# Kernel tuning notes

Measured on AMD Instinct MI355X. Metric: run time of the kernel, lower is better.

Reference implementation:

```python
import jax, jax.numpy as jnp
import numpy as np

D_MODEL = 1024
N_HEADS = 16
HEAD_DIM = D_MODEL // N_HEADS


def setup_inputs() -> dict:
    key = jax.random.key(0)
    ks = jax.random.split(key, 9)
    B, S = 2, 2048
    s = 1.0 / np.sqrt(D_MODEL)
    x = jax.random.normal(ks[0], (B, S, D_MODEL), dtype=jnp.float32)
    Wq = jax.random.normal(ks[1], (N_HEADS, D_MODEL, HEAD_DIM), dtype=jnp.float32) * s
    Wk = jax.random.normal(ks[2], (N_HEADS, D_MODEL, HEAD_DIM), dtype=jnp.float32) * s
    Wv = jax.random.normal(ks[3], (N_HEADS, D_MODEL, HEAD_DIM), dtype=jnp.float32) * s
    bq = jax.random.normal(ks[4], (N_HEADS, HEAD_DIM), dtype=jnp.float32) * s
    bk = jax.random.normal(ks[5], (N_HEADS, HEAD_DIM), dtype=jnp.float32) * s
    bv = jax.random.normal(ks[6], (N_HEADS, HEAD_DIM), dtype=jnp.float32) * s
    Wp = jax.random.normal(ks[7], (D_MODEL, D_MODEL), dtype=jnp.float32) * s
    bp = jax.random.normal(ks[8], (D_MODEL,), dtype=jnp.float32) * s
    return {"x": x, "Wq": Wq, "Wk": Wk, "Wv": Wv, "bq": bq, "bk": bk, "bv": bv, "Wp": Wp, "bp": bp}


def reference(x, Wq, Wk, Wv, bq, bk, bv, Wp, bp):
    # Per-head projections batched over heads: [B,S,D] x [H,D,E] -> [B,H,S,E]
    Q = jnp.einsum('bsd,hde->bhse', x, Wq) + bq[None, :, None, :]
    K = jnp.einsum('bsd,hde->bhse', x, Wk) + bk[None, :, None, :]
    V = jnp.einsum('bsd,hde->bhse', x, Wv) + bv[None, :, None, :]
    scores = jnp.einsum('bhse,bhte->bhst', Q, K) / jnp.sqrt(jnp.asarray(HEAD_DIM, x.dtype))
    attn = jax.nn.softmax(scores, axis=-1)          # [B,H,S,S]
    out = jnp.einsum('bhst,bhte->bhse', attn, V)    # [B,H,S,E]
    B, H, S, E = out.shape
    concat = out.transpose(0, 2, 1, 3).reshape(B, S, H * E)  # concat heads along feature
    return concat @ Wp.T + bp
```

## Files before the change

### kernel.cpp

```cpp
#include <hip/hip_runtime.h>
#include <hip/hip_bf16.h>

typedef __attribute__((ext_vector_type(8))) short short8;
typedef __attribute__((ext_vector_type(4))) short svec4;
typedef __attribute__((ext_vector_type(4))) float float4_t;
typedef __attribute__((ext_vector_type(8))) _Float16 half8;

#define D_MODEL 1024
#define N_HEADS 16
#define HEAD_DIM 64
#define B_SZ 2
#define SEQ 2048
#define M_ROWS (B_SZ*SEQ)
#define NQKV 3072
#define SC_LOG2E 0.18033688011112042f

__device__ __forceinline__ unsigned short f2bf(float f) {
  unsigned u = __float_as_uint(f);
  u += 0x7FFFu + ((u >> 16) & 1u);
  return (unsigned short)(u >> 16);
}

__device__ __forceinline__ unsigned short f2h(float f) {
  _Float16 h = (_Float16)f;
  return *(unsigned short*)&h;
}

__device__ __forceinline__ void gl_lds16(const unsigned short* g, unsigned short* l) {
  __builtin_amdgcn_global_load_lds(
      (const __attribute__((address_space(1))) unsigned int*)(size_t)g,
      (__attribute__((address_space(3))) unsigned int*)(unsigned int)(size_t)l,
      16, 0, 0);
}

__global__ void prep(const float* __restrict__ x, const float* __restrict__ Wp,
                     const float* __restrict__ Wq, const float* __restrict__ Wk,
                     const float* __restrict__ Wv,
                     unsigned short* __restrict__ xb, unsigned short* __restrict__ Wpb,
                     unsigned short* __restrict__ Wall) {
  __shared__ float t[16][17];
  int bid = blockIdx.x;
  if (bid < 5120) {
    const float* src; unsigned short* dst; int base;
    if (bid < 4096) { src = x;  dst = xb;  base = bid * 1024 + threadIdx.x * 4; }
    else            { src = Wp; dst = Wpb; base = (bid - 4096) * 1024 + threadIdx.x * 4; }
    float4 v = *(const float4*)(src + base);
    dst[base + 0] = f2bf(v.x);
    dst[base + 1] = f2bf(v.y);
    dst[base + 2] = f2bf(v.z);
    dst[base + 3] = f2bf(v.w);
  } else {
    int u = bid - 5120;
    int sel = u >> 12;
    u &= 4095;
    const float* W = sel == 0 ? Wq : (sel == 1 ? Wk : Wv);
    int d0 = (u & 63) * 16, e0 = ((u >> 6) & 3) * 16, hh = u >> 8;
    int tx = threadIdx.x & 15, ty = threadIdx.x >> 4;
    t[ty][tx] = W[hh * (D_MODEL * HEAD_DIM) + (d0 + ty) * HEAD_DIM + e0 + tx];
    __syncthreads();
    Wall[(size_t)(sel * 1024 + hh * 64 + e0 + ty) * D_MODEL + d0 + tx] = f2bf(t[tx][ty]);
  }
}

__global__ __launch_bounds__(256) void qkv_gemm(const unsigned short* __restrict__ xb,
                                                const unsigned short* __restrict__ Wall,
                                                const float* __restrict__ bq,
                                                const float* __restrict__ bk,
                                                const float* __restrict__ bv,
                                                unsigned short* __restrict__ Qb,
                                                unsigned short* __restrict__ Kb,
                                                unsigned short* __restrict__ Vtb) {
  __shared__ unsigned short As[128 * 32], Bs[128 * 32];
  __shared__ __align__(16) unsigned short Stage[4][16 * 72];
  const int m0 = blockIdx.x * 128, n0 = blockIdx.y * 128;
  const int lane = threadIdx.x & 63, w = threadIdx.x >> 6;
  const int l16 = lane & 15, quad = lane >> 4;
  const int wm = w & 1, wn = w >> 1;
  const int ldrow = lane >> 2, ldcol = (lane & 3) * 8;
  const unsigned short* ga0 = xb + (size_t)(m0 + w * 32 + ldrow) * D_MODEL + ldcol;
  const unsigned short* ga1 = ga0 + 16 * D_MODEL;
  const unsigned short* gb0 = Wall + (size_t)(n0 + w * 32 + ldrow) * D_MODEL + ldcol;
  const unsigned short* gb1 = gb0 + 16 * D_MODEL;
  unsigned short* lA0 = As + (w * 2 + 0) * 512;
  unsigned short* lA1 = As + (w * 2 + 1) * 512;
  unsigned short* lB0 = Bs + (w * 2 + 0) * 512;
  unsigned short* lB1 = Bs + (w * 2 + 1) * 512;
  float4_t acc[4][4];
  float4_t z = {0.f, 0.f, 0.f, 0.f};
#pragma unroll
  for (int i = 0; i < 4; i++)
#pragma unroll
    for (int j = 0; j < 4; j++) acc[i][j] = z;
  for (int k0 = 0; k0 < D_MODEL; k0 += 32) {
    __syncthreads();
    gl_lds16(ga0 + k0, lA0);
    gl_lds16(ga1 + k0, lA1);
    gl_lds16(gb0 + k0, lB0);
    gl_lds16(gb1 + k0, lB1);
    __syncthreads();
    short8 af[4], bf[4];
#pragma unroll
    for (int i = 0; i < 4; i++) af[i] = *(const short8*)&As[(wm * 64 + i * 16 + l16) * 32 + quad * 8];
#pragma unroll
    for (int j = 0; j < 4; j++) bf[j] = *(const short8*)&Bs[(wn * 64 + j * 16 + l16) * 32 + quad * 8];
#pragma unroll
    for (int i = 0; i < 4; i++)
#pragma unroll
      for (int j = 0; j < 4; j++)
        acc[i][j] = __builtin_amdgcn_mfma_f32_16x16x32_bf16(af[i], bf[j], acc[i][j], 0, 0, 0);
  }
  const int nb = n0 + wn * 64;
  const int sel = nb >> 10;
  const int h = (nb >> 6) & 15;
  const float* bias = sel == 0 ? bq : (sel == 1 ? bk : bv);
  const int mbase = m0 + wm * 64;
  const int bb = mbase >> 11;
  const size_t bh = (size_t)(bb * N_HEADS + h);
  if (sel == 2) {
    unsigned short* vs = &Stage[w][0];
    const size_t vbase = bh * (32 * 4096) + (size_t)((mbase >> 6) & 31) * 4096;
    const int e8 = lane >> 3, ch = lane & 7;
#pragma unroll
    for (int j = 0; j < 4; j++) {
      float be = bias[h * 64 + j * 16 + l16];
#pragma unroll
      for (int i = 0; i < 4; i++)
#pragma unroll
        for (int r = 0; r < 4; r++)
          vs[l16 * 72 + i * 16 + quad * 4 + r] = f2h(acc[i][j][r] + be);
#pragma unroll
      for (int rd = 0; rd < 2; rd++) {
        int er = rd * 8 + e8;
        short8 val = *(const short8*)(vs + er * 72 + ch * 8);
        *(short8*)(Vtb + vbase + (size_t)(j * 16 + er) * 64 + ch * 8) = val;
      }
    }
  } else {
    unsigned short* st = &Stage[w][0];
    unsigned short* dst = (sel == 0) ? Qb : Kb;
    const float qsc = (sel == 0) ? SC_LOG2E : 1.0f;
    const size_t rowbase = bh * SEQ + (mbase & (SEQ - 1));
    const int r2 = lane >> 1, c2 = lane & 1;
#pragma unroll
    for (int j = 0; j < 4; j++) {
      float be = bias[h * 64 + j * 16 + l16];
#pragma unroll
      for (int i = 0; i < 4; i++)
#pragma unroll
        for (int r = 0; r < 4; r++)
          st[(i * 16 + quad * 4 + r) * 18 + l16] = f2bf((acc[i][j][r] + be) * qsc);
#pragma unroll
      for (int p = 0; p < 2; p++) {
        int row = p * 32 + r2;
        short8 val = *(const short8*)(st + row * 18 + c2 * 8);
        *(short8*)(dst + (rowbase + row) * HEAD_DIM + j * 16 + c2 * 8) = val;
      }
    }
  }
}

__global__ __launch_bounds__(512) void attn_kernel(const unsigned short* __restrict__ Q,
                                                   const unsigned short* __restrict__ K,
                                                   const unsigned short* __restrict__ Vt,
                                                   unsigned short* __restrict__ concat) {
  __shared__ __align__(16) union ShU {
    unsigned short kv[2][4][64 * 64];
    struct { float4_t ot[4][4][4][16][4]; float ls[4][4][16]; } c;
  } sh;
  const int b = blockIdx.z, h = blockIdx.y;
  const int tid = threadIdx.x;
  const int lane = tid & 63, w = tid >> 6;
  const int g = w >> 2, wq = w & 3;
  const int l16 = lane & 15, quad = lane >> 4;
  const size_t bh = (size_t)(b * N_HEADS + h);
  const int q0 = blockIdx.x * 256 + wq * 64;
  const int tb = g * 1024;
  float4_t z = {0.f, 0.f, 0.f, 0.f};

  short8 aq[4][2];
#pragma unroll
  for (int rg = 0; rg < 4; rg++)
#pragma unroll
    for (int hf = 0; hf < 2; hf++)
      aq[rg][hf] = *(const short8*)(Q + (bh * SEQ + q0 + rg * 16 + l16) * HEAD_DIM + hf * 32 + quad * 8);

  const int tl = tid & 255;
  const int krow = tl >> 2, kch = (tl & 3) * 8;
  const unsigned short* kg = K + (bh * SEQ + tb + krow) * HEAD_DIM + kch;
  const int swz = (krow & 7) << 3;
  const int ktw0 = (krow * 64 + kch) ^ swz;
  const int ktw1 = (krow * 64 + kch + 32) ^ swz;
  const int vt0 = (tl & 3) * 16, vt1 = vt0 + 8;
  const unsigned short* vg = Vt + bh * (32 * 4096) + (size_t)(tb >> 6) * 4096 + krow * 64 + vt0;
  const int tp0 = ((vt0 >> 5) << 5) + (((vt0 >> 2) & 3) << 3) + (((vt0 >> 4) & 1) << 2);
  const int tp1 = ((vt1 >> 5) << 5) + (((vt1 >> 2) & 3) << 3) + (((vt1 >> 4) & 1) << 2);
  const int vtwA = (krow * 64 + tp0) ^ swz;
  const int vtwB = (krow * 64 + tp0 + 8) ^ swz;
  const int vtwC = (krow * 64 + tp1) ^ swz;
  const int vtwD = (krow * 64 + tp1 + 8) ^ swz;
  const int rsw = (l16 & 7) << 3;

  float4_t o[4][4];
#pragma unroll
  for (int rg = 0; rg < 4; rg++)
#pragma unroll
    for (int ne = 0; ne < 4; ne++) o[rg][ne] = z;
  float lsp[4] = {0.f, 0.f, 0.f, 0.f};

  short8 kreg0 = *(const short8*)kg;
  short8 kreg1 = *(const short8*)(kg + 32);
  short8 vreg0 = *(const short8*)vg;
  short8 vreg1 = *(const short8*)(vg + 8);
  kg += 4096; vg += 4096;

  auto step = [&](unsigned short* kb, unsigned short* vb, int itv) {
    *(short8*)(kb + ktw0) = kreg0;
    *(short8*)(kb + ktw1) = kreg1;
    svec4 a0 = {vreg0[0], vreg0[1], vreg0[2], vreg0[3]};
    svec4 a1 = {vreg0[4], vreg0[5], vreg0[6], vreg0[7]};
    svec4 b0 = {vreg1[0], vreg1[1], vreg1[2], vreg1[3]};
    svec4 b1 = {vreg1[4], vreg1[5], vreg1[6], vreg1[7]};
    *(svec4*)(vb + vtwA) = a0;
    *(svec4*)(vb + vtwB) = a1;
    *(svec4*)(vb + vtwC) = b0;
    *(svec4*)(vb + vtwD) = b1;
    __syncthreads();
    if (itv < 15) {
      kreg0 = *(const short8*)kg;
      kreg1 = *(const short8*)(kg + 32);
      vreg0 = *(const short8*)vg;
      vreg1 = *(const short8*)(vg + 8);
      kg += 4096; vg += 4096;
    }
#pragma unroll
    for (int p = 0; p < 2; p++) {
      float4_t s[2][4];
      __builtin_amdgcn_s_setprio(1);
#pragma unroll
      for (int tcl = 0; tcl < 2; tcl++) {
        int tc = 2 * p + tcl;
        short8 kf0 = *(const short8*)(kb + (((tc * 16 + l16) * 64 + quad * 8) ^ rsw));
        short8 kf1 = *(const short8*)(kb + (((tc * 16 + l16) * 64 + quad * 8 + 32) ^ rsw));
#pragma unroll
        for (int rg = 0; rg < 4; rg++) {
          s[tcl][rg] = __builtin_amdgcn_mfma_f32_16x16x32_bf16(kf0, aq[rg][0], z, 0, 0, 0);
          s[tcl][rg] = __builtin_amdgcn_mfma_f32_16x16x32_bf16(kf1, aq[rg][1], s[tcl][rg], 0, 0, 0);
        }
      }
      __builtin_amdgcn_s_setprio(0);
      half8 vf[4];
#pragma unroll
      for (int ne = 0; ne < 4; ne++)
        vf[ne] = *(const half8*)(vb + (((ne * 16 + l16) * 64 + p * 32 + quad * 8) ^ rsw));
#pragma unroll
      for (int rg = 0; rg < 4; rg++) {
        float pv[8];
#pragma unroll
        for (int r = 0; r < 4; r++) {
          pv[r]     = __builtin_amdgcn_exp2f(s[0][rg][r]);
          pv[4 + r] = __builtin_amdgcn_exp2f(s[1][rg][r]);
        }
        lsp[rg] += ((pv[0] + pv[1]) + (pv[2] + pv[3])) + ((pv[4] + pv[5]) + (pv[6] + pv[7]));
        half8 pa = {(_Float16)pv[0], (_Float16)pv[1], (_Float16)pv[2], (_Float16)pv[3],
                    (_Float16)pv[4], (_Float16)pv[5], (_Float16)pv[6], (_Float16)pv[7]};
        __builtin_amdgcn_s_setprio(1);
#pragma unroll
        for (int ne = 0; ne < 4; ne++)
          o[rg][ne] = __builtin_amdgcn_mfma_f32_16x16x32_f16(pa, vf[ne], o[rg][ne], 0, 0, 0);
        __builtin_amdgcn_s_setprio(0);
      }
    }
  };

  for (int it2 = 0; it2 < 8; ++it2) {
    step(sh.kv[g][0], sh.kv[g][2], 2 * it2);
    step(sh.kv[g][1], sh.kv[g][3], 2 * it2 + 1);
  }

  float lsf[4];
#pragma unroll
  for (int rg = 0; rg < 4; rg++) {
    float v = lsp[rg];
    v += __shfl_xor(v, 16, 64);
    v += __shfl_xor(v, 32, 64);
    lsf[rg] = v;
  }

  __syncthreads();
  if (g) {
#pragma unroll
    for (int rg = 0; rg < 4; rg++) {
#pragma unroll
      for (int ne = 0; ne < 4; ne++) sh.c.ot[wq][rg][ne][l16][quad] = o[rg][ne];
      if (quad == 0) sh.c.ls[wq][rg][l16] = lsf[rg];
    }
  }
  __syncthreads();
  if (!g) {
#pragma unroll
    for (int rg = 0; rg < 4; rg++) {
      float lt = lsf[rg] + sh.c.ls[wq][rg][l16];
#pragma unroll
      for (int ne = 0; ne < 4; ne++) {
        float4_t pp = sh.c.ot[wq][rg][ne][l16][quad];
        o[rg][ne] += pp;
      }
#pragma unroll
      for (int r = 0; r < 4; r++) {
        float li = 1.0f / __shfl(lt, quad * 4 + r, 64);
        int sr = q0 + rg * 16 + quad * 4 + r;
#pragma unroll
        for (int ne = 0; ne < 4; ne++)
          concat[((size_t)(b * SEQ + sr)) * D_MODEL + h * 64 + ne * 16 + l16] = f2bf(o[rg][ne][r] * li);
      }
    }
  }
}

__global__ __launch_bounds__(256) void out_gemm(const unsigned short* __restrict__ cb,
                                                const unsigned short* __restrict__ Wpb,
                                                const float* __restrict__ bp,
                                                float* __restrict__ out) {
  __shared__ unsigned short As[128 * 32], Bs[128 * 32];
  const int m0 = blockIdx.x * 128, n0 = blockIdx.y * 128;
  const int lane = threadIdx.x & 63, w = threadIdx.x >> 6;
  const int l16 = lane & 15, quad = lane >> 4;
  const int wm = w & 1, wn = w >> 1;
  const int ldrow = lane >> 2, ldcol = (lane & 3) * 8;
  const unsigned short* ga0 = cb + (size_t)(m0 + w * 32 + ldrow) * D_MODEL + ldcol;
  const unsigned short* ga1 = ga0 + 16 * D_MODEL;
  const unsigned short* gb0 = Wpb + (size_t)(n0 + w * 32 + ldrow) * D_MODEL + ldcol;
  const unsigned short* gb1 = gb0 + 16 * D_MODEL;
  unsigned short* lA0 = As + (w * 2 + 0) * 512;
  unsigned short* lA1 = As + (w * 2 + 1) * 512;
  unsigned short* lB0 = Bs + (w * 2 + 0) * 512;
  unsigned short* lB1 = Bs + (w * 2 + 1) * 512;
  float4_t acc[4][4];
  float4_t z = {0.f, 0.f, 0.f, 0.f};
#pragma unroll
  for (int i = 0; i < 4; i++)
#pragma unroll
    for (int j = 0; j < 4; j++) acc[i][j] = z;
  for (int k0 = 0; k0 < D_MODEL; k0 += 32) {
    __syncthreads();
    gl_lds16(ga0 + k0, lA0);
    gl_lds16(ga1 + k0, lA1);
    gl_lds16(gb0 + k0, lB0);
    gl_lds16(gb1 + k0, lB1);
    __syncthreads();
    short8 af[4], bf[4];
#pragma unroll
    for (int i = 0; i < 4; i++) af[i] = *(const short8*)&As[(wm * 64 + i * 16 + l16) * 32 + quad * 8];
#pragma unroll
    for (int j = 0; j < 4; j++) bf[j] = *(const short8*)&Bs[(wn * 64 + j * 16 + l16) * 32 + quad * 8];
#pragma unroll
    for (int i = 0; i < 4; i++)
#pragma unroll
      for (int j = 0; j < 4; j++)
        acc[i][j] = __builtin_amdgcn_mfma_f32_16x16x32_bf16(af[i], bf[j], acc[i][j], 0, 0, 0);
  }
#pragma unroll
  for (int i = 0; i < 4; i++)
#pragma unroll
    for (int j = 0; j < 4; j++)
#pragma unroll
      for (int r = 0; r < 4; r++) {
        int m = m0 + wm * 64 + i * 16 + quad * 4 + r;
        int oc = n0 + wn * 64 + j * 16 + l16;
        out[(size_t)m * D_MODEL + oc] = acc[i][j][r] + bp[oc];
      }
}

extern "C" void kernel_launch(void* const* d_in, const int* in_sizes, int n_in,
                              void* d_out, int out_size, void* d_ws, size_t ws_size,
                              hipStream_t stream) {
  const float* x  = (const float*)d_in[0];
  const float* Wq = (const float*)d_in[1];
  const float* Wk = (const float*)d_in[2];
  const float* Wv = (const float*)d_in[3];
  const float* bq = (const float*)d_in[4];
  const float* bk = (const float*)d_in[5];
  const float* bv = (const float*)d_in[6];
  const float* Wp = (const float*)d_in[7];
  const float* bp = (const float*)d_in[8];
  float* out = (float*)d_out;

  char* ws = (char*)d_ws;
  size_t off = 0;
  auto alloc = [&](size_t bytes) -> void* {
    void* p = ws + off;
    off += (bytes + 255) & ~(size_t)255;
    return p;
  };
  unsigned short* xb   = (unsigned short*)alloc((size_t)M_ROWS * D_MODEL * 2);
  unsigned short* Wall = (unsigned short*)alloc((size_t)NQKV * D_MODEL * 2);
  unsigned short* Wpb  = (unsigned short*)alloc((size_t)D_MODEL * D_MODEL * 2);
  unsigned short* Qb   = (unsigned short*)alloc((size_t)B_SZ * N_HEADS * SEQ * HEAD_DIM * 2);
  unsigned short* Kb   = (unsigned short*)alloc((size_t)B_SZ * N_HEADS * SEQ * HEAD_DIM * 2);
  unsigned short* Vtb  = (unsigned short*)alloc((size_t)B_SZ * N_HEADS * SEQ * HEAD_DIM * 2);
  unsigned short* cbuf = (unsigned short*)alloc((size_t)B_SZ * SEQ * D_MODEL * 2);

  prep<<<17408, 256, 0, stream>>>(x, Wp, Wq, Wk, Wv, xb, Wpb, Wall);

  qkv_gemm<<<dim3(M_ROWS / 128, NQKV / 128), 256, 0, stream>>>(xb, Wall, bq, bk, bv, Qb, Kb, Vtb);

  attn_kernel<<<dim3(SEQ / 256, N_HEADS, B_SZ), 512, 0, stream>>>(Qb, Kb, Vtb, cbuf);

  out_gemm<<<dim3(M_ROWS / 128, D_MODEL / 128), 256, 0, stream>>>(cbuf, Wpb, bp, out);
}
```

Before: 188.8 us.

## Double GEMM K-tile to 64 with XOR-swizzled LDS layout in QKV and output GEMMs

Both projection GEMMs now stage a 64-wide K slice per iteration instead of 32. This halves the number of barrier pairs and loop iterations across the K dimension. The global-to-LDS loads place each 16-byte chunk at a column XOR-swizzled by row, and the fragment reads apply the matching swizzle, to avoid LDS bank conflicts with the wider row stride. LDS use per block doubles for the A/B tiles, which may reduce occupancy. Some variables are renamed to avoid shadowing.

```diff
diff --git a/kernel.cpp b/kernel.cpp
--- a/kernel.cpp
+++ b/kernel.cpp
@@ -70,44 +70,49 @@
                                                 unsigned short* __restrict__ Qb,
                                                 unsigned short* __restrict__ Kb,
                                                 unsigned short* __restrict__ Vtb) {
-  __shared__ unsigned short As[128 * 32], Bs[128 * 32];
+  __shared__ unsigned short As[128 * 64], Bs[128 * 64];
   __shared__ __align__(16) unsigned short Stage[4][16 * 72];
   const int m0 = blockIdx.x * 128, n0 = blockIdx.y * 128;
   const int lane = threadIdx.x & 63, w = threadIdx.x >> 6;
   const int l16 = lane & 15, quad = lane >> 4;
   const int wm = w & 1, wn = w >> 1;
-  const int ldrow = lane >> 2, ldcol = (lane & 3) * 8;
-  const unsigned short* ga0 = xb + (size_t)(m0 + w * 32 + ldrow) * D_MODEL + ldcol;
-  const unsigned short* ga1 = ga0 + 16 * D_MODEL;
-  const unsigned short* gb0 = Wall + (size_t)(n0 + w * 32 + ldrow) * D_MODEL + ldcol;
-  const unsigned short* gb1 = gb0 + 16 * D_MODEL;
-  unsigned short* lA0 = As + (w * 2 + 0) * 512;
-  unsigned short* lA1 = As + (w * 2 + 1) * 512;
-  unsigned short* lB0 = Bs + (w * 2 + 0) * 512;
-  unsigned short* lB1 = Bs + (w * 2 + 1) * 512;
+  const int sr = lane >> 3;
+  const int scol = ((lane & 7) ^ sr) * 8;
+  const unsigned short* gaA = xb + (size_t)(m0 + w * 32 + sr) * D_MODEL + scol;
+  const unsigned short* gaB = Wall + (size_t)(n0 + w * 32 + sr) * D_MODEL + scol;
+  unsigned short* lA = As + (w * 32) * 64;
+  unsigned short* lB = Bs + (w * 32) * 64;
+  const int rswz = (l16 & 7);
   float4_t acc[4][4];
   float4_t z = {0.f, 0.f, 0.f, 0.f};
 #pragma unroll
   for (int i = 0; i < 4; i++)
 #pragma unroll
     for (int j = 0; j < 4; j++) acc[i][j] = z;
-  for (int k0 = 0; k0 < D_MODEL; k0 += 32) {
-    __syncthreads();
-    gl_lds16(ga0 + k0, lA0);
-    gl_lds16(ga1 + k0, lA1);
-    gl_lds16(gb0 + k0, lB0);
-    gl_lds16(gb1 + k0, lB1);
-    __syncthreads();
-    short8 af[4], bf[4];
-#pragma unroll
-    for (int i = 0; i < 4; i++) af[i] = *(const short8*)&As[(wm * 64 + i * 16 + l16) * 32 + quad * 8];
-#pragma unroll
-    for (int j = 0; j < 4; j++) bf[j] = *(const short8*)&Bs[(wn * 64 + j * 16 + l16) * 32 + quad * 8];
-#pragma unroll
-    for (int i = 0; i < 4; i++)
+  for (int k0 = 0; k0 < D_MODEL; k0 += 64) {
+    __syncthreads();
+#pragma unroll
+    for (int j = 0; j < 4; j++) {
+      gl_lds16(gaA + (size_t)j * 8 * D_MODEL + k0, lA + j * 8 * 64);
+      gl_lds16(gaB + (size_t)j * 8 * D_MODEL + k0, lB + j * 8 * 64);
+    }
+    __syncthreads();
+#pragma unroll
+    for (int kk = 0; kk < 2; kk++) {
+      const int ch = ((kk * 4 + quad) ^ rswz) * 8;
+      short8 af[4], bf[4];
+#pragma unroll
+      for (int i = 0; i < 4; i++)
+        af[i] = *(const short8*)&As[(wm * 64 + i * 16 + l16) * 64 + ch];
 #pragma unroll
       for (int j = 0; j < 4; j++)
-        acc[i][j] = __builtin_amdgcn_mfma_f32_16x16x32_bf16(af[i], bf[j], acc[i][j], 0, 0, 0);
+        bf[j] = *(const short8*)&Bs[(wn * 64 + j * 16 + l16) * 64 + ch];
+#pragma unroll
+      for (int i = 0; i < 4; i++)
+#pragma unroll
+        for (int j = 0; j < 4; j++)
+          acc[i][j] = __builtin_amdgcn_mfma_f32_16x16x32_bf16(af[i], bf[j], acc[i][j], 0, 0, 0);
+    }
   }
   const int nb = n0 + wn * 64;
   const int sel = nb >> 10;
@@ -119,7 +124,7 @@
   if (sel == 2) {
     unsigned short* vs = &Stage[w][0];
     const size_t vbase = bh * (32 * 4096) + (size_t)((mbase >> 6) & 31) * 4096;
-    const int e8 = lane >> 3, ch = lane & 7;
+    const int e8 = lane >> 3, ch2 = lane & 7;
 #pragma unroll
     for (int j = 0; j < 4; j++) {
       float be = bias[h * 64 + j * 16 + l16];
@@ -131,8 +136,8 @@
 #pragma unroll
       for (int rd = 0; rd < 2; rd++) {
         int er = rd * 8 + e8;
-        short8 val = *(const short8*)(vs + er * 72 + ch * 8);
-        *(short8*)(Vtb + vbase + (size_t)(j * 16 + er) * 64 + ch * 8) = val;
+        short8 val = *(const short8*)(vs + er * 72 + ch2 * 8);
+        *(short8*)(Vtb + vbase + (size_t)(j * 16 + er) * 64 + ch2 * 8) = val;
       }
     }
   } else {
@@ -308,10 +313,10 @@
 #pragma unroll
       for (int r = 0; r < 4; r++) {
         float li = 1.0f / __shfl(lt, quad * 4 + r, 64);
-        int sr = q0 + rg * 16 + quad * 4 + r;
+        int sr2 = q0 + rg * 16 + quad * 4 + r;
 #pragma unroll
         for (int ne = 0; ne < 4; ne++)
-          concat[((size_t)(b * SEQ + sr)) * D_MODEL + h * 64 + ne * 16 + l16] = f2bf(o[rg][ne][r] * li);
+          concat[((size_t)(b * SEQ + sr2)) * D_MODEL + h * 64 + ne * 16 + l16] = f2bf(o[rg][ne][r] * li);
       }
     }
   }
@@ -321,43 +326,48 @@
                                                 const unsigned short* __restrict__ Wpb,
                                                 const float* __restrict__ bp,
                                                 float* __restrict__ out) {
-  __shared__ unsigned short As[128 * 32], Bs[128 * 32];
+  __shared__ unsigned short As[128 * 64], Bs[128 * 64];
   const int m0 = blockIdx.x * 128, n0 = blockIdx.y * 128;
   const int lane = threadIdx.x & 63, w = threadIdx.x >> 6;
   const int l16 = lane & 15, quad = lane >> 4;
   const int wm = w & 1, wn = w >> 1;
-  const int ldrow = lane >> 2, ldcol = (lane & 3) * 8;
-  const unsigned short* ga0 = cb + (size_t)(m0 + w * 32 + ldrow) * D_MODEL + ldcol;
-  const unsigned short* ga1 = ga0 + 16 * D_MODEL;
-  const unsigned short* gb0 = Wpb + (size_t)(n0 + w * 32 + ldrow) * D_MODEL + ldcol;
-  const unsigned short* gb1 = gb0 + 16 * D_MODEL;
-  unsigned short* lA0 = As + (w * 2 + 0) * 512;
-  unsigned short* lA1 = As + (w * 2 + 1) * 512;
-  unsigned short* lB0 = Bs + (w * 2 + 0) * 512;
-  unsigned short* lB1 = Bs + (w * 2 + 1) * 512;
+  const int sr = lane >> 3;
+  const int scol = ((lane & 7) ^ sr) * 8;
+  const unsigned short* gaA = cb + (size_t)(m0 + w * 32 + sr) * D_MODEL + scol;
+  const unsigned short* gaB = Wpb + (size_t)(n0 + w * 32 + sr) * D_MODEL + scol;
+  unsigned short* lA = As + (w * 32) * 64;
+  unsigned short* lB = Bs + (w * 32) * 64;
+  const int rswz = (l16 & 7);
   float4_t acc[4][4];
   float4_t z = {0.f, 0.f, 0.f, 0.f};
 #pragma unroll
   for (int i = 0; i < 4; i++)
 #pragma unroll
     for (int j = 0; j < 4; j++) acc[i][j] = z;
-  for (int k0 = 0; k0 < D_MODEL; k0 += 32) {
-    __syncthreads();
-    gl_lds16(ga0 + k0, lA0);
-    gl_lds16(ga1 + k0, lA1);
-    gl_lds16(gb0 + k0, lB0);
-    gl_lds16(gb1 + k0, lB1);
-    __syncthreads();
-    short8 af[4], bf[4];
-#pragma unroll
-    for (int i = 0; i < 4; i++) af[i] = *(const short8*)&As[(wm * 64 + i * 16 + l16) * 32 + quad * 8];
-#pragma unroll
-    for (int j = 0; j < 4; j++) bf[j] = *(const short8*)&Bs[(wn * 64 + j * 16 + l16) * 32 + quad * 8];
-#pragma unroll
-    for (int i = 0; i < 4; i++)
+  for (int k0 = 0; k0 < D_MODEL; k0 += 64) {
+    __syncthreads();
+#pragma unroll
+    for (int j = 0; j < 4; j++) {
+      gl_lds16(gaA + (size_t)j * 8 * D_MODEL + k0, lA + j * 8 * 64);
+      gl_lds16(gaB + (size_t)j * 8 * D_MODEL + k0, lB + j * 8 * 64);
+    }
+    __syncthreads();
+#pragma unroll
+    for (int kk = 0; kk < 2; kk++) {
+      const int ch = ((kk * 4 + quad) ^ rswz) * 8;
+      short8 af[4], bf[4];
+#pragma unroll
+      for (int i = 0; i < 4; i++)
+        af[i] = *(const short8*)&As[(wm * 64 + i * 16 + l16) * 64 + ch];
 #pragma unroll
       for (int j = 0; j < 4; j++)
-        acc[i][j] = __builtin_amdgcn_mfma_f32_16x16x32_bf16(af[i], bf[j], acc[i][j], 0, 0, 0);
+        bf[j] = *(const short8*)&Bs[(wn * 64 + j * 16 + l16) * 64 + ch];
+#pragma unroll
+      for (int i = 0; i < 4; i++)
+#pragma unroll
+        for (int j = 0; j < 4; j++)
+          acc[i][j] = __builtin_amdgcn_mfma_f32_16x16x32_bf16(af[i], bf[j], acc[i][j], 0, 0, 0);
+    }
   }
 #pragma unroll
   for (int i = 0; i < 4; i++)
```

Result: no change. 189.0 us (+0.1%).
